# Kernel optimization log

Measured on AMD Instinct MI355X. Metric: run time of the kernel, lower is better.

The kernel has to match this reference:

```python
import jax, jax.numpy as jnp
import numpy as np

B = 8
NUM_CLASSES = 80
STRIDES = (8, 16, 32, 64, 128)
HS = (96, 48, 24, 12, 6)
WS = (160, 80, 40, 20, 10)
IMG_H, IMG_W = 768, 1280
OCTAVE_SCALE = 4.0
LOC_THR = 0.01
SCORE_THR = 0.05
IOU_THR = 0.5
NMS_PRE = 1000
MAX_PER_IMG = 100
MAX_RATIO_ANCHOR = abs(float(np.log(1e-6)))        # anchor_coder wh_ratio_clip=1e-6
MAX_RATIO_BBOX = abs(float(np.log(16.0 / 1000.0)))  # bbox_coder default wh_ratio_clip
CLS_OFFSET = 4096.0  # > max image coord, separates classes for class-aware NMS


def setup_inputs():
    inp = {}
    k = 0
    for i, (h, w) in enumerate(zip(HS, WS)):
        for name, c in (("cls_score", NUM_CLASSES), ("bbox_pred", 4), ("shape_pred", 2), ("loc_pred", 1)):
            k += 1
            inp[f"{name}_{i}"] = jax.random.normal(jax.random.fold_in(jax.random.key(0), k), (B, c, h, w), dtype=jnp.float32)
    return inp


def _squares(h, w, stride):
    # mmdet square anchor generator: base size stride*octave_base_scale, ratio 1, center offset 0
    xs = jnp.arange(w, dtype=jnp.float32) * stride
    ys = jnp.arange(h, dtype=jnp.float32) * stride
    yy, xx = jnp.meshgrid(ys, xs, indexing="ij")
    half = 0.5 * OCTAVE_SCALE * stride
    return jnp.stack([xx - half, yy - half, xx + half, yy + half], -1).reshape(-1, 4)


def _delta2bbox(rois, deltas, max_ratio, max_shape=None):
    dx, dy = deltas[..., 0], deltas[..., 1]
    dw = jnp.clip(deltas[..., 2], -max_ratio, max_ratio)
    dh = jnp.clip(deltas[..., 3], -max_ratio, max_ratio)
    px = (rois[..., 0] + rois[..., 2]) * 0.5
    py = (rois[..., 1] + rois[..., 3]) * 0.5
    pw = rois[..., 2] - rois[..., 0]
    ph = rois[..., 3] - rois[..., 1]
    gx = px + pw * dx
    gy = py + ph * dy
    gw = pw * jnp.exp(dw)
    gh = ph * jnp.exp(dh)
    x1, y1 = gx - 0.5 * gw, gy - 0.5 * gh
    x2, y2 = gx + 0.5 * gw, gy + 0.5 * gh
    if max_shape is not None:
        x1 = jnp.clip(x1, 0.0, float(max_shape[1]))
        x2 = jnp.clip(x2, 0.0, float(max_shape[1]))
        y1 = jnp.clip(y1, 0.0, float(max_shape[0]))
        y2 = jnp.clip(y2, 0.0, float(max_shape[0]))
    return jnp.stack([x1, y1, x2, y2], -1)


def _level(cls, bbox, shp, loc, stride, h, w):
    b = cls.shape[0]
    # NOTE: double sigmoid is faithful to the original wrapper (it sigmoids twice)
    scores = jax.nn.sigmoid(jax.nn.sigmoid(jnp.transpose(cls, (0, 2, 3, 1)).reshape(b, -1, NUM_CLASSES)))
    mask = (jax.nn.sigmoid(loc) >= LOC_THR).astype(scores.dtype)
    mask = jnp.transpose(mask, (0, 2, 3, 1)).reshape(b, -1)  # num_anchors == 1
    scores = scores * mask[:, :, None]
    deltas = jnp.transpose(shp, (0, 2, 3, 1)).reshape(b, -1, 2)
    bdel = jnp.concatenate([jnp.zeros_like(deltas), deltas], axis=-1)  # [0,0,dw,dh]
    anchors = _delta2bbox(_squares(h, w, stride)[None], bdel, MAX_RATIO_ANCHOR)  # guided anchors
    bbox = jnp.transpose(bbox, (0, 2, 3, 1)).reshape(b, -1, 4)
    n = scores.shape[1]
    if n < NMS_PRE:  # pad_with_value
        pad = NMS_PRE - n
        scores = jnp.pad(scores, ((0, 0), (0, pad), (0, 0)))
        bbox = jnp.pad(bbox, ((0, 0), (0, pad), (0, 0)))
        anchors = jnp.pad(anchors, ((0, 0), (0, pad), (0, 0)))
    _, idx = jax.lax.top_k(scores.max(-1), NMS_PRE)
    scores = jnp.take_along_axis(scores, idx[:, :, None], axis=1)
    bbox = jnp.take_along_axis(bbox, idx[:, :, None], axis=1)
    anchors = jnp.take_along_axis(anchors, idx[:, :, None], axis=1)
    proposals = _delta2bbox(anchors, bbox, MAX_RATIO_BBOX, (IMG_H, IMG_W))
    return scores, proposals


def _iou_one_vs_all(box, boxes):
    lt = jnp.maximum(box[:2], boxes[:, :2])
    rb = jnp.minimum(box[2:], boxes[:, 2:])
    wh = jnp.clip(rb - lt, 0.0, None)
    inter = wh[:, 0] * wh[:, 1]
    a1 = (box[2] - box[0]) * (box[3] - box[1])
    a2 = (boxes[:, 2] - boxes[:, 0]) * (boxes[:, 3] - boxes[:, 1])
    return inter / (a1 + a2 - inter + 1e-6)


def _nms_single(scores, boxes):
    # class-aware greedy NMS (BatchedNMS semantics): scores [N,C], boxes [N,4]
    n, c = scores.shape
    s = jnp.where(scores > SCORE_THR, scores, 0.0).reshape(-1)  # [N*C]
    offs = (jnp.arange(c, dtype=boxes.dtype) * CLS_OFFSET)[None, :, None]
    cboxes = (boxes[:, None, :] + offs).reshape(-1, 4)  # class-offset boxes

    def step(sv, _):
        i = jnp.argmax(sv)
        sc = sv[i]
        keep = sc > 0.0
        iou = _iou_one_vs_all(cboxes[i], cboxes)
        sv = jnp.where(iou > IOU_THR, 0.0, sv)  # suppresses i itself too
        cls = jnp.where(keep, (i % c).astype(jnp.int32), -1)
        return sv, (boxes[i // c], sc, cls, keep)

    _, (ob, osc, ocls, okeep) = jax.lax.scan(step, s, None, length=MAX_PER_IMG)
    kf = okeep.astype(boxes.dtype)
    return okeep.sum().astype(jnp.int32), ob * kf[:, None], osc * kf, ocls


def _forward(tensors):
    mlvl_scores, mlvl_props = [], []
    for i in range(5):
        s, p = _level(tensors[4 * i], tensors[4 * i + 1], tensors[4 * i + 2], tensors[4 * i + 3],
                      STRIDES[i], HS[i], WS[i])
        mlvl_scores.append(s)
        mlvl_props.append(p)
    scores = jnp.concatenate(mlvl_scores, axis=1)   # [B, 5000, 80]
    props = jnp.concatenate(mlvl_props, axis=1)     # [B, 5000, 4]
    k = min(max(1000, NMS_PRE), scores.shape[1])
    _, idx = jax.lax.top_k(scores.max(-1), k)
    scores = jnp.take_along_axis(scores, idx[:, :, None], axis=1)
    props = jnp.take_along_axis(props, idx[:, :, None], axis=1)
    return jax.vmap(_nms_single)(scores, props)


def reference(cls_score_0, bbox_pred_0, shape_pred_0, loc_pred_0,
              cls_score_1, bbox_pred_1, shape_pred_1, loc_pred_1,
              cls_score_2, bbox_pred_2, shape_pred_2, loc_pred_2,
              cls_score_3, bbox_pred_3, shape_pred_3, loc_pred_3,
              cls_score_4, bbox_pred_4, shape_pred_4, loc_pred_4):
    tensors = [cls_score_0, bbox_pred_0, shape_pred_0, loc_pred_0,
               cls_score_1, bbox_pred_1, shape_pred_1, loc_pred_1,
               cls_score_2, bbox_pred_2, shape_pred_2, loc_pred_2,
               cls_score_3, bbox_pred_3, shape_pred_3, loc_pred_3,
               cls_score_4, bbox_pred_4, shape_pred_4, loc_pred_4]
    num_detected, proposals, out_scores, cls_id = _forward(tensors)
    return num_detected, proposals, out_scores, cls_id
```

## Files before the change

kernel.cpp:

```cpp
#include <hip/hip_runtime.h>
#include <stdint.h>

#define NCLS 80
#define BATCH 8
#define NA 20460
#define TOPK 1000
#define MAXPER 100
#define CAP 8
#define POOL 256
#define IMG_WF 1280.0f
#define IMG_HF 768.0f
#define CLS_OFF 4096.0f
#define MAX_RATIO_ANCHOR 13.815510557964274f
#define MAX_RATIO_BBOX   4.1351665567423557f

#define K2_HALF_UP (0.5 + 0x1p-25)

__constant__ int   c_lvoff[6]  = {0, 15360, 19200, 20160, 20400, 20460};
__constant__ int   c_lvoff4[6] = {0, 3840, 4800, 5040, 5100, 5115};
__constant__ int   c_lw[5]    = {160, 80, 40, 20, 10};
__constant__ int   c_lh[5]    = {96, 48, 24, 12, 6};
__constant__ float c_ls[5]    = {8.f, 16.f, 32.f, 64.f, 128.f};

struct InPtrs {
  const float* cls[5];
  const float* bbox[5];
  const float* shp[5];
  const float* loc[5];
};

__device__ __forceinline__ float sigf(float x) { return 1.0f / (1.0f + expf(-x)); }

__device__ __forceinline__ int wave_red_sum_i32(int v) {
  int t;
  t = __builtin_amdgcn_update_dpp(0, v, 0x111, 0xf, 0xf, false); v += t;
  t = __builtin_amdgcn_update_dpp(0, v, 0x112, 0xf, 0xf, false); v += t;
  t = __builtin_amdgcn_update_dpp(0, v, 0x114, 0xf, 0xf, false); v += t;
  t = __builtin_amdgcn_update_dpp(0, v, 0x118, 0xf, 0xf, false); v += t;
  t = __builtin_amdgcn_update_dpp(0, v, 0x142, 0xf, 0xf, false); v += t;
  t = __builtin_amdgcn_update_dpp(0, v, 0x143, 0xf, 0xf, false); v += t;
  return __builtin_amdgcn_readlane(v, 63);
}
__device__ __forceinline__ void wave_red_top2(unsigned m1, unsigned m2,
                                              unsigned& r1, unsigned& r2) {
#define T2STEP(ctrl) { \
    unsigned o1 = (unsigned)__builtin_amdgcn_update_dpp(0, (int)m1, ctrl, 0xf, 0xf, false); \
    unsigned o2 = (unsigned)__builtin_amdgcn_update_dpp(0, (int)m2, ctrl, 0xf, 0xf, false); \
    unsigned tm = min(m1, o1); \
    m1 = max(m1, o1); \
    m2 = max(tm, max(m2, o2)); }
  T2STEP(0x111) T2STEP(0x112) T2STEP(0x114) T2STEP(0x118) T2STEP(0x142) T2STEP(0x143)
#undef T2STEP
  r1 = (unsigned)__builtin_amdgcn_readlane((int)m1, 63);
  r2 = (unsigned)__builtin_amdgcn_readlane((int)m2, 63);
}

__global__ __launch_bounds__(256) void k_maxscore(InPtrs P, float* maxscore) {
  int gid = blockIdx.x * 256 + threadIdx.x;
  if (gid >= BATCH * (NA / 4)) return;
  int b = gid / (NA / 4);
  int q = gid - b * (NA / 4);
  int l = 0;
  while (q >= c_lvoff4[l + 1]) ++l;
  int hw = c_lh[l] * c_lw[l];
  int sp = (q - c_lvoff4[l]) * 4;
  const float4* cls = (const float4*)(P.cls[l] + (size_t)(b * NCLS) * hw + sp);
  int s4 = hw >> 2;
  float4 m = cls[0];
  for (int c = 1; c < NCLS; ++c) {
    float4 v = cls[(size_t)c * s4];
    m.x = fmaxf(m.x, v.x); m.y = fmaxf(m.y, v.y);
    m.z = fmaxf(m.z, v.z); m.w = fmaxf(m.w, v.w);
  }
  float4 lo = *(const float4*)(P.loc[l] + (size_t)b * hw + sp);
  float4 r;
  r.x = (sigf(lo.x) >= 0.01f) ? sigf(sigf(m.x)) : 0.0f;
  r.y = (sigf(lo.y) >= 0.01f) ? sigf(sigf(m.y)) : 0.0f;
  r.z = (sigf(lo.z) >= 0.01f) ? sigf(sigf(m.z)) : 0.0f;
  r.w = (sigf(lo.w) >= 0.01f) ? sigf(sigf(m.w)) : 0.0f;
  ((float4*)maxscore)[(size_t)b * (NA / 4) + q] = r;
}

__global__ __launch_bounds__(1024) void k_select(const float* maxscore, int* sel) {
  int b = blockIdx.x;
  const unsigned int* ms = (const unsigned int*)(maxscore + (size_t)b * NA);
  int tid = threadIdx.x;
  int wv = tid >> 6;
  int lane = tid & 63;
  __shared__ unsigned s_h[2048];
  __shared__ int s_wtot[16];
  __shared__ int s_res[2];
  __shared__ unsigned long long s_A[1024];
  __shared__ unsigned long long s_B[1024];

  unsigned w[20];
  #pragma unroll
  for (int k = 0; k < 5; ++k) {
    int q = tid * 5 + k;
    uint4 u = (q < NA / 4) ? ((const uint4*)ms)[q] : make_uint4(0u, 0u, 0u, 0u);
    w[k * 4 + 0] = u.x & 0x3FFFFFu;
    w[k * 4 + 1] = u.y & 0x3FFFFFu;
    w[k * 4 + 2] = u.z & 0x3FFFFFu;
    w[k * 4 + 3] = u.w & 0x3FFFFFu;
  }
  int lim = NA - tid * 20;
  lim = (lim < 0) ? 0 : ((lim > 20) ? 20 : lim);

  s_h[tid] = 0u; s_h[tid + 1024] = 0u;
  __syncthreads();

  auto scanFind = [&](int target) {
    int b0 = 2047 - 2 * tid;
    int h0 = (int)s_h[b0];
    int h1 = (int)s_h[b0 - 1];
    int pair = h0 + h1;
    int incl = pair;
    #pragma unroll
    for (int o = 1; o < 64; o <<= 1) {
      int uu = __shfl_up(incl, o, 64);
      if (lane >= o) incl += uu;
    }
    if (lane == 63) s_wtot[wv] = incl;
    __syncthreads();
    int woff = 0;
    #pragma unroll
    for (int ww = 0; ww < 16; ++ww) woff += (ww < wv) ? s_wtot[ww] : 0;
    int excl = woff + incl - pair;
    if (excl < target && excl + h0 >= target) { s_res[0] = b0; s_res[1] = excl; }
    int e1 = excl + h0;
    if (e1 < target && e1 + h1 >= target) { s_res[0] = b0 - 1; s_res[1] = e1; }
    __syncthreads();
  };

  #pragma unroll
  for (int k = 0; k < 20; ++k) atomicAdd(&s_h[w[k] >> 11], 1u);
  __syncthreads();
  scanFind(TOPK);
  int B1 = s_res[0];
  int NGT1 = s_res[1];

  s_h[tid] = 0u; s_h[tid + 1024] = 0u;
  __syncthreads();
  #pragma unroll
  for (int k = 0; k < 20; ++k)
    if ((int)(w[k] >> 11) == B1) atomicAdd(&s_h[w[k] & 0x7FFu], 1u);
  __syncthreads();
  scanFind(TOPK - NGT1);
  unsigned V = ((unsigned)B1 << 11) | (unsigned)s_res[0];

  if (tid < 1024 - TOPK) s_A[TOPK + tid] = 0ull;

  int cgt = 0;
  #pragma unroll
  for (int k = 0; k < 20; ++k) cgt += (w[k] > V) ? 1 : 0;
  {
    int incl = cgt;
    #pragma unroll
    for (int o = 1; o < 64; o <<= 1) {
      int uu = __shfl_up(incl, o, 64);
      if (lane >= o) incl += uu;
    }
    if (lane == 63) s_wtot[wv] = incl;
    __syncthreads();
    int woff = 0, tot = 0;
    #pragma unroll
    for (int ww = 0; ww < 16; ++ww) { tot += s_wtot[ww]; woff += (ww < wv) ? s_wtot[ww] : 0; }
    int pos = woff + incl - cgt;
    #pragma unroll
    for (int k = 0; k < 20; ++k) {
      if (w[k] > V) {
        int i = tid * 20 + k;
        s_A[pos++] = ((unsigned long long)w[k] << 32) |
                     (unsigned long long)(0xFFFFFFFFu - (unsigned)i);
      }
    }
    int ngt = tot;
    int need = TOPK - ngt;
    __syncthreads();

    int ceq = 0;
    #pragma unroll
    for (int k = 0; k < 20; ++k) if (k < lim && w[k] == V) ++ceq;
    int incl2 = ceq;
    #pragma unroll
    for (int o = 1; o < 64; o <<= 1) {
      int uu = __shfl_up(incl2, o, 64);
      if (lane >= o) incl2 += uu;
    }
    if (lane == 63) s_wtot[wv] = incl2;
    __syncthreads();
    int woff2 = 0;
    #pragma unroll
    for (int ww = 0; ww < 16; ++ww) woff2 += (ww < wv) ? s_wtot[ww] : 0;
    int r = woff2 + incl2 - ceq;
    #pragma unroll
    for (int k = 0; k < 20; ++k) {
      if (k < lim && w[k] == V) {
        if (r < need) {
          int i = tid * 20 + k;
          s_A[ngt + r] = ((unsigned long long)V << 32) |
                         (unsigned long long)(0xFFFFFFFFu - (unsigned)i);
        }
        ++r;
      }
    }
  }
  __syncthreads();

  unsigned long long key = s_A[tid];
  int tog = 0;
  for (unsigned k = 2; k <= 1024; k <<= 1) {
    for (unsigned j = k >> 1; j > 0; j >>= 1) {
      unsigned long long other;
      if (j >= 64) {
        unsigned long long* cur = tog ? s_A : s_B;
        cur[tid] = key;
        __syncthreads();
        other = cur[tid ^ (int)j];
        tog ^= 1;
      } else {
        other = __shfl_xor(key, (int)j, 64);
      }
      bool takeMax = (((tid & (int)k) == 0) == ((tid & (int)j) == 0));
      unsigned long long mx = (key > other) ? key : other;
      unsigned long long mn = (key > other) ? other : key;
      key = takeMax ? mx : mn;
    }
  }
  if (tid < TOPK) {
    sel[b * TOPK + tid] = (int)(0xFFFFFFFFu - (unsigned)(key & 0xFFFFFFFFull));
  }
}

__global__ __launch_bounds__(256) void k_gather(InPtrs P, const int* sel, float* boxes, float* sv) {
  int wvi = threadIdx.x >> 6;
  int lane = threadIdx.x & 63;
  int wid = blockIdx.x * 4 + wvi;
  int b = wid / TOPK;
  int r = wid - b * TOPK;
  __shared__ float s_sc[4][NCLS];

  int a = sel[b * TOPK + r];
  int l = 0;
  while (a >= c_lvoff[l + 1]) ++l;
  int within = a - c_lvoff[l];
  int W = c_lw[l], H = c_lh[l];
  int y = within / W, x = within - y * W;
  int hw = H * W;
  int sp = within;
  float stride = c_ls[l];
  float px = (float)x * stride;
  float py = (float)y * stride;
  float pw = 4.0f * stride;

  const float* shp = P.shp[l];
  float dws = shp[(b * 2 + 0) * hw + sp];
  float dhs = shp[(b * 2 + 1) * hw + sp];
  dws = fminf(fmaxf(dws, -MAX_RATIO_ANCHOR), MAX_RATIO_ANCHOR);
  dhs = fminf(fmaxf(dhs, -MAX_RATIO_ANCHOR), MAX_RATIO_ANCHOR);
  float gw = pw * expf(dws);
  float gh = pw * expf(dhs);
  float ax1 = px - 0.5f * gw, ax2 = px + 0.5f * gw;
  float ay1 = py - 0.5f * gh, ay2 = py + 0.5f * gh;

  const float* bb = P.bbox[l];
  float dx = bb[(b * 4 + 0) * hw + sp];
  float dy = bb[(b * 4 + 1) * hw + sp];
  float dw = bb[(b * 4 + 2) * hw + sp];
  float dh = bb[(b * 4 + 3) * hw + sp];
  dw = fminf(fmaxf(dw, -MAX_RATIO_BBOX), MAX_RATIO_BBOX);
  dh = fminf(fmaxf(dh, -MAX_RATIO_BBOX), MAX_RATIO_BBOX);
  float px2 = (ax1 + ax2) * 0.5f, py2 = (ay1 + ay2) * 0.5f;
  float pw2 = ax2 - ax1, ph2 = ay2 - ay1;
  float gx = px2 + pw2 * dx, gy = py2 + ph2 * dy;
  float gw2 = pw2 * expf(dw), gh2 = ph2 * expf(dh);
  float x1 = fminf(fmaxf(gx - 0.5f * gw2, 0.0f), IMG_WF);
  float x2 = fminf(fmaxf(gx + 0.5f * gw2, 0.0f), IMG_WF);
  float y1 = fminf(fmaxf(gy - 0.5f * gh2, 0.0f), IMG_HF);
  float y2 = fminf(fmaxf(gy + 0.5f * gh2, 0.0f), IMG_HF);
  if (lane == 0) {
    float4 st; st.x = x1; st.y = y1; st.z = x2; st.w = y2;
    ((float4*)boxes)[b * TOPK + r] = st;
  }

  const float* cls = P.cls[l];
  float sl = sigf(P.loc[l][b * hw + sp]);
  bool mask = (sl >= 0.01f);
  int base = (b * NCLS) * hw + sp;
  for (int c = lane; c < NCLS; c += 64) {
    float vv = 0.0f;
    if (mask) {
      float s2 = sigf(sigf(cls[base + c * hw]));
      vv = (s2 > 0.05f) ? s2 : 0.0f;
    }
    s_sc[wvi][c] = vv;
  }
  __syncthreads();
  int t = threadIdx.x;
  if (t < NCLS) {
    int r0 = blockIdx.x * 4 - b * TOPK;
    float4 o; o.x = s_sc[0][t]; o.y = s_sc[1][t]; o.z = s_sc[2][t]; o.w = s_sc[3][t];
    *(float4*)(sv + ((size_t)(b * NCLS + t) * TOPK + r0)) = o;
  }
}

__global__ __launch_bounds__(256) void k_nms(const float* boxes, const float* sv,
                                             float* keptScore, int* keptRow, int* kc,
                                             const int* flags, const int* gbits, int cap) {
  int bc = blockIdx.x;
  if (flags && flags[bc] == 0) return;
  int b = bc / NCLS;
  int c = bc - b * NCLS;
  int tid = threadIdx.x;
  int wv = tid >> 6, lane = tid & 63;

  unsigned Glow = 0u;
  if (gbits) Glow = ((unsigned)gbits[b]) & 0x3FFFFFu;

  __shared__ float4 s_box[TOPK];
  __shared__ float  s_ard[TOPK];
  __shared__ unsigned long long s_p2[2][4];

  float x1[4], y1[4], x2[4], y2[4], ar[4];
  unsigned key[4];
  float off = (float)c * CLS_OFF;
  const float* svc = sv + (size_t)(b * NCLS + c) * TOPK;
  #pragma unroll
  for (int j = 0; j < 4; ++j) {
    int row = j * 256 + tid;
    if (row < TOPK) {
      float4 bo = ((const float4*)boxes)[b * TOPK + row];
      float a = bo.x + off, d = bo.y + off, e = bo.z + off, f = bo.w + off;
      x1[j] = a; y1[j] = d; x2[j] = e; y2[j] = f;
      ar[j] = (e - a) * (f - d);
      unsigned bits = __float_as_uint(svc[row]);
      key[j] = ((bits & 0x3FFFFFu) << 10) | (1023u - (unsigned)row);
      float sden = ar[j] + 1e-6f;
      bool deg = !((double)ar[j] > (double)sden * K2_HALF_UP);
      float4 sb; sb.x = a; sb.y = d; sb.z = e; sb.w = f;
      s_box[row] = sb;
      s_ard[row] = __uint_as_float(__float_as_uint(ar[j]) | (deg ? 0x80000000u : 0u));
    } else {
      x1[j] = y1[j] = x2[j] = y2[j] = ar[j] = 0.0f;
      key[j] = 0u;
    }
  }
  __syncthreads();

  int kept = 0;
  bool sticky = false;
  float* ks = keptScore + (size_t)(b * NCLS + c) * MAXPER;
  int*   kr = keptRow   + (size_t)(b * NCLS + c) * MAXPER;

  for (int round = 0; round < cap; ++round) {
    int par = round & 1;
    unsigned hi1 = max(key[0], key[1]), lo1 = min(key[0], key[1]);
    unsigned hi2 = max(key[2], key[3]), lo2 = min(key[2], key[3]);
    unsigned m1 = max(hi1, hi2);
    unsigned m2 = max(min(hi1, hi2), max(lo1, lo2));
    unsigned w1, w2;
    wave_red_top2(m1, m2, w1, w2);
    if (lane == 0) s_p2[par][wv] = ((unsigned long long)w1 << 32) | w2;
    __syncthreads();
    unsigned k0 = 0u, k1 = 0u;
    #pragma unroll
    for (int w = 0; w < 4; ++w) {
      unsigned long long pp = s_p2[par][w];
      unsigned p1 = (unsigned)(pp >> 32), p2 = (unsigned)pp;
      unsigned tm = min(k0, p1);
      k0 = max(k0, p1);
      k1 = max(tm, max(k1, p2));
    }
    if (k0 < 1024u) break;
    if ((k0 >> 10) < Glow) break;
    int brow1 = 1023 - (int)(k0 & 1023u);
    float bs1 = __uint_as_float(0x3F000000u | (k0 >> 10));
    float4 bb1 = s_box[brow1];
    unsigned au1 = __float_as_uint(s_ard[brow1]);
    bool deg1 = (au1 >> 31) != 0u;
    float ba1 = __uint_as_float(au1 & 0x7FFFFFFFu);
    if (tid == 0) { ks[kept] = bs1; kr[kept] = brow1; }
    kept++;
    if (deg1) { sticky = true; break; }
    if (kept >= cap) break;
    bool live2 = (k1 >= 1024u) && ((k1 >> 10) >= Glow);
    if (!live2) break;
    bool do2 = false, deg2 = false;
    float4 bb2; float ba2 = 0.0f;
    {
      int brow2 = 1023 - (int)(k1 & 1023u);
      float bs2 = __uint_as_float(0x3F000000u | (k1 >> 10));
      bb2 = s_box[brow2];
      unsigned au2 = __float_as_uint(s_ard[brow2]);
      deg2 = (au2 >> 31) != 0u;
      ba2 = __uint_as_float(au2 & 0x7FFFFFFFu);
      float ltx = fmaxf(bb1.x, bb2.x), rbx = fminf(bb1.z, bb2.z);
      float lty = fmaxf(bb1.y, bb2.y), rby = fminf(bb1.w, bb2.w);
      float w_ = fmaxf(rbx - ltx, 0.0f), h_ = fmaxf(rby - lty, 0.0f);
      float inter = w_ * h_;
      float denom = ((ba1 + ba2) - inter) + 1e-6f;
      if (!((double)inter > (double)denom * K2_HALF_UP)) {
        do2 = true;
        if (tid == 0) { ks[kept] = bs2; kr[kept] = brow2; }
        kept++;
      }
    }
    if (do2 && deg2) { sticky = true; break; }
    #pragma unroll
    for (int j = 0; j < 4; ++j) {
      {
        float ltx = fmaxf(bb1.x, x1[j]), rbx = fminf(bb1.z, x2[j]);
        float lty = fmaxf(bb1.y, y1[j]), rby = fminf(bb1.w, y2[j]);
        float w_ = fmaxf(rbx - ltx, 0.0f), h_ = fmaxf(rby - lty, 0.0f);
        float inter = w_ * h_;
        float denom = ((ba1 + ar[j]) - inter) + 1e-6f;
        if ((double)inter > (double)denom * K2_HALF_UP) key[j] = 0u;
      }
      if (do2) {
        float ltx = fmaxf(bb2.x, x1[j]), rbx = fminf(bb2.z, x2[j]);
        float lty = fmaxf(bb2.y, y1[j]), rby = fminf(bb2.w, y2[j]);
        float w_ = fmaxf(rbx - ltx, 0.0f), h_ = fmaxf(rby - lty, 0.0f);
        float inter = w_ * h_;
        float denom = ((ba2 + ar[j]) - inter) + 1e-6f;
        if ((double)inter > (double)denom * K2_HALF_UP) key[j] = 0u;
      }
    }
    if (kept >= cap) break;
  }
  if (tid == 0) kc[b * NCLS + c] = sticky ? -kept : kept;
}

__global__ __launch_bounds__(256) void k_cut(const float* keptScore, const int* kc,
                                             int* flags, int* gbits) {
  int b = blockIdx.x;
  int tid = threadIdx.x;
  int wv = tid >> 6, lane = tid & 63;
  __shared__ int s_abs[NCLS];
  __shared__ int s_neg[NCLS];
  __shared__ unsigned s_h[2048];
  __shared__ int s_wtot[4];
  __shared__ int s_res[2];
  __shared__ int s_tot[4];

  if (tid < NCLS) {
    int v = kc[b * NCLS + tid];
    s_abs[tid] = (v < 0) ? -v : v;
    s_neg[tid] = (v < 0) ? 1 : 0;
  }
  #pragma unroll
  for (int j = 0; j < 8; ++j) s_h[tid * 8 + j] = 0u;
  __syncthreads();

  unsigned vv[3] = {0u, 0u, 0u};
  #pragma unroll
  for (int t = 0; t < 3; ++t) {
    int e = tid + t * 256;
    if (e < NCLS * CAP) {
      int c = e / CAP, k = e - c * CAP;
      if (k < s_abs[c])
        vv[t] = __float_as_uint(keptScore[(size_t)b * NCLS * MAXPER + c * MAXPER + k])
                & 0x3FFFFFu;
    }
  }
  int live = ((vv[0] != 0u) ? 1 : 0) + ((vv[1] != 0u) ? 1 : 0) + ((vv[2] != 0u) ? 1 : 0);
  live = wave_red_sum_i32(live);
  if (lane == 0) s_tot[wv] = live;
  #pragma unroll
  for (int t = 0; t < 3; ++t) if (vv[t]) atomicAdd(&s_h[vv[t] >> 11], 1u);
  __syncthreads();
  int T = s_tot[0] + s_tot[1] + s_tot[2] + s_tot[3];

  auto scanFind = [&](int target) {
    int base = 2047 - 8 * tid;
    int h[8]; int loc = 0;
    #pragma unroll
    for (int j = 0; j < 8; ++j) { h[j] = (int)s_h[base - j]; loc += h[j]; }
    int incl = loc;
    #pragma unroll
    for (int o = 1; o < 64; o <<= 1) {
      int uu = __shfl_up(incl, o, 64);
      if (lane >= o) incl += uu;
    }
    if (lane == 63) s_wtot[wv] = incl;
    __syncthreads();
    int woff = 0;
    #pragma unroll
    for (int ww = 0; ww < 4; ++ww) woff += (ww < wv) ? s_wtot[ww] : 0;
    int e = woff + incl - loc;
    #pragma unroll
    for (int j = 0; j < 8; ++j) {
      if (e < target && e + h[j] >= target) { s_res[0] = base - j; s_res[1] = e; }
      e += h[j];
    }
    __syncthreads();
  };

  unsigned G = 0u;
  if (T >= MAXPER) {
    scanFind(MAXPER);
    int B1 = s_res[0], NGT1 = s_res[1];
    #pragma unroll
    for (int j = 0; j < 8; ++j) s_h[tid * 8 + j] = 0u;
    __syncthreads();
    #pragma unroll
    for (int t = 0; t < 3; ++t)
      if (vv[t] && (int)(vv[t] >> 11) == B1) atomicAdd(&s_h[vv[t] & 0x7FFu], 1u);
    __syncthreads();
    scanFind(MAXPER - NGT1);
    G = 0x3F000000u | ((unsigned)B1 << 11) | (unsigned)s_res[0];
  }
  if (tid == 0) gbits[b] = (int)G;
  if (tid < NCLS) {
    int f = 0;
    if (s_abs[tid] == CAP && !s_neg[tid]) {
      unsigned slast = __float_as_uint(
          keptScore[(size_t)b * NCLS * MAXPER + tid * MAXPER + (CAP - 1)]);
      if (slast >= G) f = 1;
    }
    flags[b * NCLS + tid] = f;
  }
}

__global__ __launch_bounds__(256) void k_merge(const float* boxes, const float* keptScore,
                                               const int* keptRow, const int* kc, float* out) {
  int b = blockIdx.x;
  int tid = threadIdx.x;
  int wv = tid >> 6, lane = tid & 63;
  __shared__ int s_kc[NCLS];
  __shared__ unsigned s_h[2048];
  __shared__ int s_wtot[4];
  __shared__ int s_res[2];
  __shared__ int s_tot[4];
  __shared__ int s_pos;
  __shared__ int s_sticky;
  __shared__ int s_navail;
  __shared__ unsigned long long s_pool[POOL];
  __shared__ unsigned long long s_sorted[POOL];

  for (int c = tid; c < NCLS; c += 256) s_kc[c] = kc[b * NCLS + c];
  if (tid == 0) { s_pos = 0; s_sticky = 0x7FFFFFFF; s_navail = 0; }
  for (int i = tid; i < POOL; i += 256) { s_pool[i] = 0ull; s_sorted[i] = 0ull; }
  #pragma unroll
  for (int j = 0; j < 8; ++j) s_h[tid * 8 + j] = 0u;
  __syncthreads();

  unsigned sc[32];
  #pragma unroll
  for (int s = 0; s < 32; ++s) {
    int i = tid + s * 256;
    unsigned vvv = 0u;
    if (i < NCLS * MAXPER) {
      int c = i / MAXPER, k = i - c * MAXPER;
      int kcv = s_kc[c];
      int ka = (kcv < 0) ? -kcv : kcv;
      if (k < ka)
        vvv = __float_as_uint(keptScore[(size_t)b * NCLS * MAXPER + i]) & 0x3FFFFFu;
    }
    sc[s] = vvv;
  }
  int live = 0;
  #pragma unroll
  for (int s = 0; s < 32; ++s) live += (sc[s] != 0u) ? 1 : 0;
  live = wave_red_sum_i32(live);
  if (lane == 0) s_tot[wv] = live;
  #pragma unroll
  for (int s = 0; s < 32; ++s) if (sc[s]) atomicAdd(&s_h[sc[s] >> 11], 1u);
  __syncthreads();
  int T = s_tot[0] + s_tot[1] + s_tot[2] + s_tot[3];

  auto scanFind = [&](int target) {
    int base = 2047 - 8 * tid;
    int h[8]; int loc = 0;
    #pragma unroll
    for (int j = 0; j < 8; ++j) { h[j] = (int)s_h[base - j]; loc += h[j]; }
    int incl = loc;
    #pragma unroll
    for (int o = 1; o < 64; o <<= 1) {
      int uu = __shfl_up(incl, o, 64);
      if (lane >= o) incl += uu;
    }
    if (lane == 63) s_wtot[wv] = incl;
    __syncthreads();
    int woff = 0;
    #pragma unroll
    for (int ww = 0; ww < 4; ++ww) woff += (ww < wv) ? s_wtot[ww] : 0;
    int e = woff + incl - loc;
    #pragma unroll
    for (int j = 0; j < 8; ++j) {
      if (e < target && e + h[j] >= target) { s_res[0] = base - j; s_res[1] = e; }
      e += h[j];
    }
    __syncthreads();
  };

  unsigned V = 1u;
  if (T > MAXPER) {
    scanFind(MAXPER);
    int B1 = s_res[0], NGT1 = s_res[1];
    #pragma unroll
    for (int j = 0; j < 8; ++j) s_h[tid * 8 + j] = 0u;
    __syncthreads();
    #pragma unroll
    for (int s = 0; s < 32; ++s)
      if (sc[s] && (int)(sc[s] >> 11) == B1) atomicAdd(&s_h[sc[s] & 0x7FFu], 1u);
    __syncthreads();
    scanFind(MAXPER - NGT1);
    V = ((unsigned)B1 << 11) | (unsigned)s_res[0];
  }

  #pragma unroll
  for (int s = 0; s < 32; ++s) {
    if (sc[s] >= V && sc[s] != 0u) {
      int i = tid + s * 256;
      int c = i / MAXPER, k = i - c * MAXPER;
      int kcv = s_kc[c];
      int ka = (kcv < 0) ? -kcv : kcv;
      unsigned st = (kcv < 0 && k == ka - 1) ? 1u : 0u;
      unsigned row = (unsigned)keptRow[(size_t)b * NCLS * MAXPER + i];
      unsigned flat = row * 80u + (unsigned)c;
      int p = atomicAdd(&s_pos, 1);
      if (p < POOL)
        s_pool[p] = ((unsigned long long)(0x3F000000u | sc[s]) << 32) |
                    (unsigned long long)(0x7FFFFFFFu - ((flat << 1) | st));
    }
  }
  __syncthreads();

  if (tid < POOL) {
    unsigned long long mykey = s_pool[tid];
    if (mykey != 0ull) {
      int rank = 0;
      #pragma unroll 8
      for (int s = 0; s < POOL; ++s) rank += (s_pool[s] > mykey) ? 1 : 0;
      s_sorted[rank] = mykey;
    }
  }
  __syncthreads();

  if (tid < MAXPER) {
    unsigned long long key = s_sorted[tid];
    if (key != 0ull) {
      atomicAdd(&s_navail, 1);
      if ((((unsigned)key) & 1u) == 0u) atomicMin(&s_sticky, tid);
    }
  }
  __syncthreads();
  int navail = s_navail;
  int p = s_sticky;
  int n = (p < navail) ? MAXPER : navail;

  if (tid == 0) out[b] = (float)n;
  const int OB = BATCH;
  const int OP = OB + BATCH * MAXPER * 4;
  const int OS = OP + BATCH * MAXPER;
  if (tid < MAXPER) {
    int k = tid;
    float bx0 = 0.f, bx1 = 0.f, bx2 = 0.f, bx3 = 0.f, scf = 0.f, cf = -1.0f;
    if (k < n) {
      int idx = (k > p) ? p : k;
      unsigned long long key = s_sorted[idx];
      unsigned flat = (0x7FFFFFFFu - (unsigned)key) >> 1;
      unsigned cls = flat % 80u;
      unsigned row = flat / 80u;
      float4 bo = ((const float4*)boxes)[b * TOPK + row];
      bx0 = bo.x; bx1 = bo.y; bx2 = bo.z; bx3 = bo.w;
      scf = __uint_as_float((unsigned)(key >> 32));
      cf = (float)cls;
    }
    float* po = out + OB + (size_t)(b * MAXPER + k) * 4;
    po[0] = bx0; po[1] = bx1; po[2] = bx2; po[3] = bx3;
    out[OP + b * MAXPER + k] = scf;
    out[OS + b * MAXPER + k] = cf;
  }
}

extern "C" void kernel_launch(void* const* d_in, const int* in_sizes, int n_in,
                              void* d_out, int out_size, void* d_ws, size_t ws_size,
                              hipStream_t stream) {
  InPtrs P;
  for (int l = 0; l < 5; ++l) {
    P.cls[l]  = (const float*)d_in[4 * l + 0];
    P.bbox[l] = (const float*)d_in[4 * l + 1];
    P.shp[l]  = (const float*)d_in[4 * l + 2];
    P.loc[l]  = (const float*)d_in[4 * l + 3];
  }
  float* maxscore  = (float*)d_ws;
  int*   sel       = (int*)(maxscore + BATCH * NA);
  float* boxes     = (float*)(sel + BATCH * TOPK);
  float* sv        = boxes + BATCH * TOPK * 4;
  float* keptScore = sv + BATCH * NCLS * TOPK;
  int*   keptRow   = (int*)(keptScore + BATCH * NCLS * MAXPER);
  int*   kc        = keptRow + BATCH * NCLS * MAXPER;
  int*   flags     = kc + BATCH * NCLS;
  int*   gbits     = flags + BATCH * NCLS;
  float* out = (float*)d_out;

  k_maxscore<<<(BATCH * (NA / 4) + 255) / 256, 256, 0, stream>>>(P, maxscore);
  k_select<<<BATCH, 1024, 0, stream>>>(maxscore, sel);
  k_gather<<<BATCH * TOPK / 4, 256, 0, stream>>>(P, sel, boxes, sv);
  k_nms<<<BATCH * NCLS, 256, 0, stream>>>(boxes, sv, keptScore, keptRow, kc,
                                          (const int*)nullptr, (const int*)nullptr, CAP);
  k_cut<<<BATCH, 256, 0, stream>>>(keptScore, kc, flags, gbits);
  k_nms<<<BATCH * NCLS, 256, 0, stream>>>(boxes, sv, keptScore, keptRow, kc,
                                          flags, gbits, MAXPER);
  k_merge<<<BATCH, 256, 0, stream>>>(boxes, keptScore, keptRow, kc, out);
}
```

Before: 203.6 us.

## Split class-max reduction into four class chunks and finish it in select

```diff
diff --git a/kernel.cpp b/kernel.cpp
--- a/kernel.cpp
+++ b/kernel.cpp
@@ -8,6 +8,7 @@
 #define MAXPER 100
 #define CAP 8
 #define POOL 256
+#define CCHUNK 4
 #define IMG_WF 1280.0f
 #define IMG_HF 768.0f
 #define CLS_OFF 4096.0f
@@ -55,8 +56,10 @@
   r2 = (unsigned)__builtin_amdgcn_readlane((int)m2, 63);
 }
 
-__global__ __launch_bounds__(256) void k_maxscore(InPtrs P, float* maxscore) {
-  int gid = blockIdx.x * 256 + threadIdx.x;
+__global__ __launch_bounds__(256) void k_part(InPtrs P, float* partial) {
+  const int bpc = (BATCH * (NA / 4) + 255) / 256;
+  int chunk = blockIdx.x / bpc;
+  int gid = (blockIdx.x - chunk * bpc) * 256 + threadIdx.x;
   if (gid >= BATCH * (NA / 4)) return;
   int b = gid / (NA / 4);
   int q = gid - b * (NA / 4);
@@ -64,26 +67,20 @@
   while (q >= c_lvoff4[l + 1]) ++l;
   int hw = c_lh[l] * c_lw[l];
   int sp = (q - c_lvoff4[l]) * 4;
-  const float4* cls = (const float4*)(P.cls[l] + (size_t)(b * NCLS) * hw + sp);
+  const int c0 = chunk * (NCLS / CCHUNK);
+  const float4* cls = (const float4*)(P.cls[l] + (size_t)(b * NCLS + c0) * hw + sp);
   int s4 = hw >> 2;
   float4 m = cls[0];
-  for (int c = 1; c < NCLS; ++c) {
+  for (int c = 1; c < NCLS / CCHUNK; ++c) {
     float4 v = cls[(size_t)c * s4];
     m.x = fmaxf(m.x, v.x); m.y = fmaxf(m.y, v.y);
     m.z = fmaxf(m.z, v.z); m.w = fmaxf(m.w, v.w);
   }
-  float4 lo = *(const float4*)(P.loc[l] + (size_t)b * hw + sp);
-  float4 r;
-  r.x = (sigf(lo.x) >= 0.01f) ? sigf(sigf(m.x)) : 0.0f;
-  r.y = (sigf(lo.y) >= 0.01f) ? sigf(sigf(m.y)) : 0.0f;
-  r.z = (sigf(lo.z) >= 0.01f) ? sigf(sigf(m.z)) : 0.0f;
-  r.w = (sigf(lo.w) >= 0.01f) ? sigf(sigf(m.w)) : 0.0f;
-  ((float4*)maxscore)[(size_t)b * (NA / 4) + q] = r;
-}
-
-__global__ __launch_bounds__(1024) void k_select(const float* maxscore, int* sel) {
+  ((float4*)partial)[((size_t)chunk * BATCH + b) * (NA / 4) + q] = m;
+}
+
+__global__ __launch_bounds__(1024) void k_select(InPtrs P, const float* partial, int* sel) {
   int b = blockIdx.x;
-  const unsigned int* ms = (const unsigned int*)(maxscore + (size_t)b * NA);
   int tid = threadIdx.x;
   int wv = tid >> 6;
   int lane = tid & 63;
@@ -93,15 +90,36 @@
   __shared__ unsigned long long s_A[1024];
   __shared__ unsigned long long s_B[1024];
 
+  const int NAq = NA / 4;
   unsigned w[20];
   #pragma unroll
   for (int k = 0; k < 5; ++k) {
     int q = tid * 5 + k;
-    uint4 u = (q < NA / 4) ? ((const uint4*)ms)[q] : make_uint4(0u, 0u, 0u, 0u);
-    w[k * 4 + 0] = u.x & 0x3FFFFFu;
-    w[k * 4 + 1] = u.y & 0x3FFFFFu;
-    w[k * 4 + 2] = u.z & 0x3FFFFFu;
-    w[k * 4 + 3] = u.w & 0x3FFFFFu;
+    float4 r = make_float4(0.f, 0.f, 0.f, 0.f);
+    if (q < NAq) {
+      float4 p0 = ((const float4*)partial)[((size_t)0 * BATCH + b) * NAq + q];
+      float4 p1 = ((const float4*)partial)[((size_t)1 * BATCH + b) * NAq + q];
+      float4 p2 = ((const float4*)partial)[((size_t)2 * BATCH + b) * NAq + q];
+      float4 p3 = ((const float4*)partial)[((size_t)3 * BATCH + b) * NAq + q];
+      float4 m;
+      m.x = fmaxf(fmaxf(p0.x, p1.x), fmaxf(p2.x, p3.x));
+      m.y = fmaxf(fmaxf(p0.y, p1.y), fmaxf(p2.y, p3.y));
+      m.z = fmaxf(fmaxf(p0.z, p1.z), fmaxf(p2.z, p3.z));
+      m.w = fmaxf(fmaxf(p0.w, p1.w), fmaxf(p2.w, p3.w));
+      int l = 0;
+      while (q >= c_lvoff4[l + 1]) ++l;
+      int hw = c_lh[l] * c_lw[l];
+      int sp = (q - c_lvoff4[l]) * 4;
+      float4 lo = *(const float4*)(P.loc[l] + (size_t)b * hw + sp);
+      r.x = (sigf(lo.x) >= 0.01f) ? sigf(sigf(m.x)) : 0.0f;
+      r.y = (sigf(lo.y) >= 0.01f) ? sigf(sigf(m.y)) : 0.0f;
+      r.z = (sigf(lo.z) >= 0.01f) ? sigf(sigf(m.z)) : 0.0f;
+      r.w = (sigf(lo.w) >= 0.01f) ? sigf(sigf(m.w)) : 0.0f;
+    }
+    w[k * 4 + 0] = __float_as_uint(r.x) & 0x3FFFFFu;
+    w[k * 4 + 1] = __float_as_uint(r.y) & 0x3FFFFFu;
+    w[k * 4 + 2] = __float_as_uint(r.z) & 0x3FFFFFu;
+    w[k * 4 + 3] = __float_as_uint(r.w) & 0x3FFFFFu;
   }
   int lim = NA - tid * 20;
   lim = (lim < 0) ? 0 : ((lim > 20) ? 20 : lim);
@@ -684,8 +702,8 @@
     P.shp[l]  = (const float*)d_in[4 * l + 2];
     P.loc[l]  = (const float*)d_in[4 * l + 3];
   }
-  float* maxscore  = (float*)d_ws;
-  int*   sel       = (int*)(maxscore + BATCH * NA);
+  float* partial   = (float*)d_ws;
+  int*   sel       = (int*)(partial + CCHUNK * BATCH * NA);
   float* boxes     = (float*)(sel + BATCH * TOPK);
   float* sv        = boxes + BATCH * TOPK * 4;
   float* keptScore = sv + BATCH * NCLS * TOPK;
@@ -695,8 +713,9 @@
   int*   gbits     = flags + BATCH * NCLS;
   float* out = (float*)d_out;
 
-  k_maxscore<<<(BATCH * (NA / 4) + 255) / 256, 256, 0, stream>>>(P, maxscore);
-  k_select<<<BATCH, 1024, 0, stream>>>(maxscore, sel);
+  const int bpc = (BATCH * (NA / 4) + 255) / 256;
+  k_part<<<CCHUNK * bpc, 256, 0, stream>>>(P, partial);
+  k_select<<<BATCH, 1024, 0, stream>>>(P, partial, sel);
   k_gather<<<BATCH * TOPK / 4, 256, 0, stream>>>(P, sel, boxes, sv);
   k_nms<<<BATCH * NCLS, 256, 0, stream>>>(boxes, sv, keptScore, keptRow, kc,
                                           (const int*)nullptr, (const int*)nullptr, CAP);
```

Result: no change. 203.6 us (+0.0%).
